# Performance work log

Hardware: AMD Instinct MI355X
Metric: run time of the kernel (lower is better)

## Reference

```python
import jax, jax.numpy as jnp
import numpy as np

NUM_EXPERTS = 8
TOP_K = 2
DIM = 1024
HIDDEN = 4096
B, S = 2, 1024


def setup_inputs() -> dict:
    key = jax.random.key(0)
    k_x, k_g, k_1, k_2, k_3 = jax.random.split(key, 5)
    s_d = 1.0 / np.sqrt(DIM)
    s_h = 1.0 / np.sqrt(HIDDEN)
    return {
        "x": jax.random.normal(k_x, (B, S, DIM), dtype=jnp.float32),
        "gate_w": jax.random.normal(k_g, (NUM_EXPERTS, DIM), dtype=jnp.float32) * s_d,
        "w1": jax.random.normal(k_1, (NUM_EXPERTS, HIDDEN, DIM), dtype=jnp.float32) * s_d,
        "w2": jax.random.normal(k_2, (NUM_EXPERTS, DIM, HIDDEN), dtype=jnp.float32) * s_h,
        "w3": jax.random.normal(k_3, (NUM_EXPERTS, HIDDEN, DIM), dtype=jnp.float32) * s_d,
    }


def reference(x, gate_w, w1, w2, w3):
    orig_shape = x.shape
    xt = x.reshape(-1, orig_shape[-1])                      # [T, D]
    scores = xt @ gate_w.T                                  # [T, E] (gate_softmax=False)
    top_vals, top_idx = jax.lax.top_k(scores, TOP_K)        # [T, K]
    top_w = jax.nn.softmax(top_vals, axis=-1)               # [T, K]
    # per-token combine weights over experts: [T, E]
    combine = jnp.einsum("tke,tk->te", jax.nn.one_hot(top_idx, NUM_EXPERTS, dtype=xt.dtype), top_w)
    # dense per-expert SwiGLU FFN; combine masks out unrouted experts
    h = jax.nn.silu(jnp.einsum("td,ehd->eth", xt, w1)) * jnp.einsum("td,ehd->eth", xt, w3)
    ye = jnp.einsum("eth,edh->etd", h, w2)                  # [E, T, D]
    y = jnp.einsum("te,etd->td", combine, ye)               # [T, D]
    return y.reshape(orig_shape)
```

## Files before the change

kernel.cpp:

```cpp
#include <hip/hip_runtime.h>
#include <hip/hip_bf16.h>

#define NUM_EXPERTS 8
#define TOPK 2
#define DIM 1024
#define HIDDEN 4096
#define T_TOKENS 2048
#define TOTAL_ROWS (T_TOKENS * TOPK)
#define LDSP 40

typedef __bf16 bf16x8 __attribute__((ext_vector_type(8)));
typedef float f32x4 __attribute__((ext_vector_type(4)));

__device__ __forceinline__ unsigned short f2bf(float f) {
  unsigned int u = __float_as_uint(f);
  u += 0x7FFF + ((u >> 16) & 1);
  return (unsigned short)(u >> 16);
}

__device__ __forceinline__ void gl_lds16(const void* g, void* l) {
  __builtin_amdgcn_global_load_lds(
      (const __attribute__((address_space(1))) unsigned int*)g,
      (__attribute__((address_space(3))) unsigned int*)l, 16, 0, 0);
}

#define WAIT_VM(N) __builtin_amdgcn_s_waitcnt(0x0F70 | (N))
#define BARRIER() __builtin_amdgcn_s_barrier()

__global__ __launch_bounds__(256) void cast_kernel(
    const float* __restrict__ src, unsigned short* __restrict__ dst, int n8) {
  int i = blockIdx.x * blockDim.x + threadIdx.x;
  int stride = gridDim.x * blockDim.x;
  for (; i < n8; i += stride) {
    float4 a = ((const float4*)src)[i * 2];
    float4 b = ((const float4*)src)[i * 2 + 1];
    ushort4 o0, o1;
    o0.x = f2bf(a.x); o0.y = f2bf(a.y); o0.z = f2bf(a.z); o0.w = f2bf(a.w);
    o1.x = f2bf(b.x); o1.y = f2bf(b.y); o1.z = f2bf(b.z); o1.w = f2bf(b.w);
    ((ushort4*)dst)[i * 2] = o0;
    ((ushort4*)dst)[i * 2 + 1] = o1;
  }
}

__global__ __launch_bounds__(256) void gate_kernel(
    const float* __restrict__ x, const float* __restrict__ gw,
    int* __restrict__ tok_idx, float* __restrict__ tok_w) {
  int wid = threadIdx.x >> 6;
  int lane = threadIdx.x & 63;
  int t = blockIdx.x * 4 + wid;
  if (t >= T_TOKENS) return;

  float xv[16];
#pragma unroll
  for (int i = 0; i < 16; i++) xv[i] = x[t * DIM + lane + i * 64];

  float s[NUM_EXPERTS];
#pragma unroll
  for (int e = 0; e < NUM_EXPERTS; e++) {
    float acc = 0.f;
#pragma unroll
    for (int i = 0; i < 16; i++) acc += xv[i] * gw[e * DIM + lane + i * 64];
#pragma unroll
    for (int off = 32; off; off >>= 1) acc += __shfl_xor(acc, off, 64);
    s[e] = acc;
  }
  if (lane == 0) {
    int i0 = 0;
    float v0 = s[0];
#pragma unroll
    for (int e = 1; e < NUM_EXPERTS; e++)
      if (s[e] > v0) { v0 = s[e]; i0 = e; }
    int i1 = -1;
    float v1 = -1e30f;
#pragma unroll
    for (int e = 0; e < NUM_EXPERTS; e++)
      if (e != i0 && s[e] > v1) { v1 = s[e]; i1 = e; }
    float e1 = __expf(v1 - v0);
    float d = 1.f + e1;
    tok_idx[t * 2] = i0;
    tok_idx[t * 2 + 1] = i1;
    tok_w[t * 2] = 1.f / d;
    tok_w[t * 2 + 1] = e1 / d;
  }
}

__global__ void scatter_kernel(const int* __restrict__ tok_idx,
                               const float* __restrict__ tok_w,
                               int* __restrict__ row_token,
                               float* __restrict__ row_weight,
                               int* __restrict__ counts,
                               int* __restrict__ offsets) {
  __shared__ int sc[NUM_EXPERTS];
  int tid = threadIdx.x;
  if (tid < NUM_EXPERTS) sc[tid] = 0;
  __syncthreads();
  for (int i = tid; i < TOTAL_ROWS; i += blockDim.x)
    atomicAdd(&sc[tok_idx[i]], 1);
  __syncthreads();
  if (tid == 0) {
    int run = 0;
    for (int e = 0; e < NUM_EXPERTS; e++) {
      int c = sc[e];
      counts[e] = c;
      offsets[e] = run;
      sc[e] = run;
      run += c;
    }
  }
  __syncthreads();
  for (int i = tid; i < TOTAL_ROWS; i += blockDim.x) {
    int e = tok_idx[i];
    int pos = atomicAdd(&sc[e], 1);
    row_token[pos] = i >> 1;
    row_weight[pos] = tok_w[i];
  }
}


__global__ __launch_bounds__(256) void ffn1_fast(
    const unsigned short* __restrict__ xb, const unsigned short* __restrict__ w1b,
    const unsigned short* __restrict__ w3b, const int* __restrict__ row_token,
    const int* __restrict__ counts, const int* __restrict__ offsets,
    unsigned short* __restrict__ hbuf) {
  int e = blockIdx.z;
  int cnt = counts[e];
  int m0 = blockIdx.y * 128;
  if (m0 >= cnt) return;
  int n0 = blockIdx.x * 128;
  int row_base = offsets[e];

  __shared__ __align__(16) unsigned short lA[2][128 * 32];
  __shared__ __align__(16) unsigned short lB1[2][128 * 32];
  __shared__ __align__(16) unsigned short lB3[2][128 * 32];

  int tid = threadIdx.x;
  int lane = tid & 63, wid = tid >> 6;
  int quad = lane >> 4, l16 = lane & 15;
  int wm = wid >> 1, wn = wid & 1;

  long aoff[2];
  long boff[2];
#pragma unroll
  for (int it = 0; it < 2; it++) {
    int c = it * 256 + tid;
    int r = c >> 2, seg = c & 3;
    int t = (m0 + r) < cnt ? row_token[row_base + m0 + r] : 0;
    aoff[it] = (long)t * DIM + seg * 8;
    boff[it] = (long)r * DIM + seg * 8;
  }
  const unsigned short* w1p = w1b + (long)e * HIDDEN * DIM + (long)n0 * DIM;
  const unsigned short* w3p = w3b + (long)e * HIDDEN * DIM + (long)n0 * DIM;

  f32x4 acc1[4][4], acc3[4][4];
#pragma unroll
  for (int mi = 0; mi < 4; mi++)
#pragma unroll
    for (int ni = 0; ni < 4; ni++) {
      acc1[mi][ni] = (f32x4){0.f, 0.f, 0.f, 0.f};
      acc3[mi][ni] = (f32x4){0.f, 0.f, 0.f, 0.f};
    }

#pragma unroll
  for (int it = 0; it < 2; it++) {
    int c = it * 256 + tid;
    gl_lds16(xb + aoff[it], &lA[0][c * 8]);
    gl_lds16(w1p + boff[it], &lB1[0][c * 8]);
    gl_lds16(w3p + boff[it], &lB3[0][c * 8]);
  }

  int pc = 0;
  for (int k0 = 0; k0 < DIM; k0 += 32, pc ^= 1) {
    BARRIER();
    if (k0 + 32 < DIM) {
      int nb = pc ^ 1, kn = k0 + 32;
#pragma unroll
      for (int it = 0; it < 2; it++) {
        int c = it * 256 + tid;
        gl_lds16(xb + aoff[it] + kn, &lA[nb][c * 8]);
        gl_lds16(w1p + boff[it] + kn, &lB1[nb][c * 8]);
        gl_lds16(w3p + boff[it] + kn, &lB3[nb][c * 8]);
      }
      WAIT_VM(6);
    } else {
      WAIT_VM(0);
    }
    BARRIER();

    bf16x8 af[4], b1f[4], b3f[4];
#pragma unroll
    for (int i = 0; i < 4; i++) {
      af[i]  = *(const bf16x8*)(const void*)&lA[pc][(wm * 64 + i * 16 + l16) * 32 + quad * 8];
      b1f[i] = *(const bf16x8*)(const void*)&lB1[pc][(wn * 64 + i * 16 + l16) * 32 + quad * 8];
      b3f[i] = *(const bf16x8*)(const void*)&lB3[pc][(wn * 64 + i * 16 + l16) * 32 + quad * 8];
    }
#pragma unroll
    for (int mi = 0; mi < 4; mi++)
#pragma unroll
      for (int ni = 0; ni < 4; ni++) {
        acc1[mi][ni] = __builtin_amdgcn_mfma_f32_16x16x32_bf16(af[mi], b1f[ni], acc1[mi][ni], 0, 0, 0);
        acc3[mi][ni] = __builtin_amdgcn_mfma_f32_16x16x32_bf16(af[mi], b3f[ni], acc3[mi][ni], 0, 0, 0);
      }
  }

#pragma unroll
  for (int mi = 0; mi < 4; mi++) {
#pragma unroll
    for (int r = 0; r < 4; r++) {
      int m = wm * 64 + mi * 16 + quad * 4 + r;
      if (m0 + m < cnt) {
        long rowoff = (long)(row_base + m0 + m) * HIDDEN;
#pragma unroll
        for (int ni = 0; ni < 4; ni++) {
          int n = n0 + wn * 64 + ni * 16 + l16;
          float v1 = acc1[mi][ni][r];
          float v3 = acc3[mi][ni][r];
          float sig = 1.f / (1.f + __expf(-v1));
          hbuf[rowoff + n] = f2bf(v1 * sig * v3);
        }
      }
    }
  }
}

__global__ __launch_bounds__(256) void ffn2_fast(
    const unsigned short* __restrict__ hbuf, const unsigned short* __restrict__ w2b,
    const int* __restrict__ row_token, const float* __restrict__ row_weight,
    const int* __restrict__ counts, const int* __restrict__ offsets,
    float* __restrict__ y) {
  int e = blockIdx.z;
  int cnt = counts[e];
  int mt = blockIdx.y >> 1, kh = blockIdx.y & 1;
  int m0 = mt * 128;
  if (m0 >= cnt) return;
  int n0 = blockIdx.x * 128;
  int row_base = offsets[e];
  const int KHALF = HIDDEN / 2;
  int kbeg = kh * KHALF;

  __shared__ __align__(16) unsigned short lA[2][128 * 32];
  __shared__ __align__(16) unsigned short lB[2][128 * 32];

  int tid = threadIdx.x;
  int lane = tid & 63, wid = tid >> 6;
  int quad = lane >> 4, l16 = lane & 15;
  int wm = wid >> 1, wn = wid & 1;

  long aoff[2], boff[2];
#pragma unroll
  for (int it = 0; it < 2; it++) {
    int c = it * 256 + tid;
    int r = c >> 2, seg = c & 3;
    int row = (m0 + r) < cnt ? (row_base + m0 + r) : row_base;
    aoff[it] = (long)row * HIDDEN + seg * 8 + kbeg;
    boff[it] = (long)r * HIDDEN + seg * 8 + kbeg;
  }
  const unsigned short* w2p = w2b + (long)e * DIM * HIDDEN + (long)n0 * HIDDEN;

  f32x4 acc[4][4];
#pragma unroll
  for (int mi = 0; mi < 4; mi++)
#pragma unroll
    for (int ni = 0; ni < 4; ni++) acc[mi][ni] = (f32x4){0.f, 0.f, 0.f, 0.f};

#pragma unroll
  for (int it = 0; it < 2; it++) {
    int c = it * 256 + tid;
    gl_lds16(hbuf + aoff[it], &lA[0][c * 8]);
    gl_lds16(w2p + boff[it], &lB[0][c * 8]);
  }

  int pc = 0;
  for (int k0 = 0; k0 < KHALF; k0 += 32, pc ^= 1) {
    BARRIER();
    if (k0 + 32 < KHALF) {
      int nb = pc ^ 1, kn = k0 + 32;
#pragma unroll
      for (int it = 0; it < 2; it++) {
        int c = it * 256 + tid;
        gl_lds16(hbuf + aoff[it] + kn, &lA[nb][c * 8]);
        gl_lds16(w2p + boff[it] + kn, &lB[nb][c * 8]);
      }
      WAIT_VM(4);
    } else {
      WAIT_VM(0);
    }
    BARRIER();

    bf16x8 af[4], bfr[4];
#pragma unroll
    for (int i = 0; i < 4; i++) {
      af[i]  = *(const bf16x8*)(const void*)&lA[pc][(wm * 64 + i * 16 + l16) * 32 + quad * 8];
      bfr[i] = *(const bf16x8*)(const void*)&lB[pc][(wn * 64 + i * 16 + l16) * 32 + quad * 8];
    }
#pragma unroll
    for (int mi = 0; mi < 4; mi++)
#pragma unroll
      for (int ni = 0; ni < 4; ni++)
        acc[mi][ni] = __builtin_amdgcn_mfma_f32_16x16x32_bf16(af[mi], bfr[ni], acc[mi][ni], 0, 0, 0);
  }

#pragma unroll
  for (int mi = 0; mi < 4; mi++) {
#pragma unroll
    for (int r = 0; r < 4; r++) {
      int m = wm * 64 + mi * 16 + quad * 4 + r;
      if (m0 + m < cnt) {
        int t = row_token[row_base + m0 + m];
        float wgt = row_weight[row_base + m0 + m];
        long yoff = (long)t * DIM + n0 + wn * 64;
#pragma unroll
        for (int ni = 0; ni < 4; ni++)
          atomicAdd(&y[yoff + ni * 16 + l16], wgt * acc[mi][ni][r]);
      }
    }
  }
}


__global__ __launch_bounds__(256) void ffn1_slow(
    const float* __restrict__ x, const float* __restrict__ w1,
    const float* __restrict__ w3, const int* __restrict__ row_token,
    const int* __restrict__ counts, const int* __restrict__ offsets,
    unsigned short* __restrict__ hbuf) {
  int e = blockIdx.z;
  int cnt = counts[e];
  int m0 = blockIdx.y * 128;
  if (m0 >= cnt) return;
  int n0 = blockIdx.x * 128;
  int row_base = offsets[e];

  __shared__ __align__(16) unsigned short lA[128 * LDSP];
  __shared__ __align__(16) unsigned short lB1[128 * LDSP];
  __shared__ __align__(16) unsigned short lB3[128 * LDSP];

  int tid = threadIdx.x;
  int lane = tid & 63, wid = tid >> 6;
  int quad = lane >> 4, l16 = lane & 15;
  int wm = wid >> 1, wn = wid & 1;

  long aoff[4];
  bool aval[4];
#pragma unroll
  for (int it = 0; it < 4; it++) {
    int linear = it * 256 + tid;
    int r = linear >> 3, c4 = linear & 7;
    bool v = (m0 + r) < cnt;
    aval[it] = v;
    int t = v ? row_token[row_base + m0 + r] : 0;
    aoff[it] = (long)t * DIM + c4 * 4;
  }
  const float* w1p = w1 + (long)e * HIDDEN * DIM;
  const float* w3p = w3 + (long)e * HIDDEN * DIM;

  f32x4 acc1[4][4], acc3[4][4];
#pragma unroll
  for (int mi = 0; mi < 4; mi++)
#pragma unroll
    for (int ni = 0; ni < 4; ni++) {
      acc1[mi][ni] = (f32x4){0.f, 0.f, 0.f, 0.f};
      acc3[mi][ni] = (f32x4){0.f, 0.f, 0.f, 0.f};
    }

  for (int k0 = 0; k0 < DIM; k0 += 32) {
#pragma unroll
    for (int it = 0; it < 4; it++) {
      int linear = it * 256 + tid;
      int r = linear >> 3, c4 = linear & 7;
      float4 v = make_float4(0.f, 0.f, 0.f, 0.f);
      if (aval[it]) v = *(const float4*)(x + aoff[it] + k0);
      ushort4 b;
      b.x = f2bf(v.x); b.y = f2bf(v.y); b.z = f2bf(v.z); b.w = f2bf(v.w);
      *(ushort4*)&lA[r * LDSP + c4 * 4] = b;
    }
#pragma unroll
    for (int it = 0; it < 4; it++) {
      int linear = it * 256 + tid;
      int r = linear >> 3, c4 = linear & 7;
      long boff = (long)(n0 + r) * DIM + k0 + c4 * 4;
      float4 v1 = *(const float4*)(w1p + boff);
      float4 v3 = *(const float4*)(w3p + boff);
      ushort4 b1, b3;
      b1.x = f2bf(v1.x); b1.y = f2bf(v1.y); b1.z = f2bf(v1.z); b1.w = f2bf(v1.w);
      b3.x = f2bf(v3.x); b3.y = f2bf(v3.y); b3.z = f2bf(v3.z); b3.w = f2bf(v3.w);
      *(ushort4*)&lB1[r * LDSP + c4 * 4] = b1;
      *(ushort4*)&lB3[r * LDSP + c4 * 4] = b3;
    }
    __syncthreads();

    bf16x8 af[4], b1f[4], b3f[4];
#pragma unroll
    for (int i = 0; i < 4; i++) {
      af[i]  = *(const bf16x8*)(const void*)&lA[(wm * 64 + i * 16 + l16) * LDSP + quad * 8];
      b1f[i] = *(const bf16x8*)(const void*)&lB1[(wn * 64 + i * 16 + l16) * LDSP + quad * 8];
      b3f[i] = *(const bf16x8*)(const void*)&lB3[(wn * 64 + i * 16 + l16) * LDSP + quad * 8];
    }
#pragma unroll
    for (int mi = 0; mi < 4; mi++)
#pragma unroll
      for (int ni = 0; ni < 4; ni++) {
        acc1[mi][ni] = __builtin_amdgcn_mfma_f32_16x16x32_bf16(af[mi], b1f[ni], acc1[mi][ni], 0, 0, 0);
        acc3[mi][ni] = __builtin_amdgcn_mfma_f32_16x16x32_bf16(af[mi], b3f[ni], acc3[mi][ni], 0, 0, 0);
      }
    __syncthreads();
  }

#pragma unroll
  for (int mi = 0; mi < 4; mi++) {
#pragma unroll
    for (int r = 0; r < 4; r++) {
      int m = wm * 64 + mi * 16 + quad * 4 + r;
      if (m0 + m < cnt) {
        long rowoff = (long)(row_base + m0 + m) * HIDDEN;
#pragma unroll
        for (int ni = 0; ni < 4; ni++) {
          int n = n0 + wn * 64 + ni * 16 + l16;
          float v1 = acc1[mi][ni][r];
          float v3 = acc3[mi][ni][r];
          float sig = 1.f / (1.f + __expf(-v1));
          hbuf[rowoff + n] = f2bf(v1 * sig * v3);
        }
      }
    }
  }
}

__global__ __launch_bounds__(256) void ffn2_slow(
    const unsigned short* __restrict__ hbuf, const float* __restrict__ w2,
    const int* __restrict__ row_token, const float* __restrict__ row_weight,
    const int* __restrict__ counts, const int* __restrict__ offsets,
    float* __restrict__ y) {
  int e = blockIdx.z;
  int cnt = counts[e];
  int m0 = blockIdx.y * 128;
  if (m0 >= cnt) return;
  int n0 = blockIdx.x * 128;
  int row_base = offsets[e];

  __shared__ __align__(16) unsigned short lA[128 * LDSP];
  __shared__ __align__(16) unsigned short lB[128 * LDSP];

  int tid = threadIdx.x;
  int lane = tid & 63, wid = tid >> 6;
  int quad = lane >> 4, l16 = lane & 15;
  int wm = wid >> 1, wn = wid & 1;

  const float* w2p = w2 + (long)e * DIM * HIDDEN;

  f32x4 acc[4][4];
#pragma unroll
  for (int mi = 0; mi < 4; mi++)
#pragma unroll
    for (int ni = 0; ni < 4; ni++) acc[mi][ni] = (f32x4){0.f, 0.f, 0.f, 0.f};

  for (int k0 = 0; k0 < HIDDEN; k0 += 32) {
#pragma unroll
    for (int it = 0; it < 2; it++) {
      int linear = it * 256 + tid;
      int r = linear >> 2, c8 = linear & 3;
      float4 v = make_float4(0.f, 0.f, 0.f, 0.f);
      if (m0 + r < cnt)
        v = *(const float4*)(hbuf + (long)(row_base + m0 + r) * HIDDEN + k0 + c8 * 8);
      *(float4*)&lA[r * LDSP + c8 * 8] = v;
    }
#pragma unroll
    for (int it = 0; it < 4; it++) {
      int linear = it * 256 + tid;
      int r = linear >> 3, c4 = linear & 7;
      float4 v = *(const float4*)(w2p + (long)(n0 + r) * HIDDEN + k0 + c4 * 4);
      ushort4 b;
      b.x = f2bf(v.x); b.y = f2bf(v.y); b.z = f2bf(v.z); b.w = f2bf(v.w);
      *(ushort4*)&lB[r * LDSP + c4 * 4] = b;
    }
    __syncthreads();

    bf16x8 af[4], bfr[4];
#pragma unroll
    for (int i = 0; i < 4; i++) {
      af[i]  = *(const bf16x8*)(const void*)&lA[(wm * 64 + i * 16 + l16) * LDSP + quad * 8];
      bfr[i] = *(const bf16x8*)(const void*)&lB[(wn * 64 + i * 16 + l16) * LDSP + quad * 8];
    }
#pragma unroll
    for (int mi = 0; mi < 4; mi++)
#pragma unroll
      for (int ni = 0; ni < 4; ni++)
        acc[mi][ni] = __builtin_amdgcn_mfma_f32_16x16x32_bf16(af[mi], bfr[ni], acc[mi][ni], 0, 0, 0);
    __syncthreads();
  }

#pragma unroll
  for (int mi = 0; mi < 4; mi++) {
#pragma unroll
    for (int r = 0; r < 4; r++) {
      int m = wm * 64 + mi * 16 + quad * 4 + r;
      if (m0 + m < cnt) {
        int t = row_token[row_base + m0 + m];
        float wgt = row_weight[row_base + m0 + m];
        long yoff = (long)t * DIM + n0 + wn * 64;
#pragma unroll
        for (int ni = 0; ni < 4; ni++)
          atomicAdd(&y[yoff + ni * 16 + l16], wgt * acc[mi][ni][r]);
      }
    }
  }
}

extern "C" void kernel_launch(void* const* d_in, const int* in_sizes, int n_in,
                              void* d_out, int out_size, void* d_ws, size_t ws_size,
                              hipStream_t stream) {
  const float* x = (const float*)d_in[0];
  const float* gw = (const float*)d_in[1];
  const float* w1 = (const float*)d_in[2];
  const float* w2 = (const float*)d_in[3];
  const float* w3 = (const float*)d_in[4];
  float* y = (float*)d_out;

  char* ws = (char*)d_ws;
  int* row_token = (int*)ws;
  float* row_weight = (float*)(ws + 16384);
  int* counts = (int*)(ws + 32768);
  int* offsets = (int*)(ws + 32768 + 32);
  int* tok_idx = (int*)(ws + 32896);
  float* tok_w = (float*)(ws + 32896 + 16384);
  const size_t HBUF_OFF = 65664;
  const size_t XB_OFF   = HBUF_OFF + 33554432ull;
  const size_t W1B_OFF  = XB_OFF + 4194304ull;
  const size_t W2B_OFF  = W1B_OFF + 67108864ull;
  const size_t W3B_OFF  = W2B_OFF + 67108864ull;
  const size_t NEED     = W3B_OFF + 67108864ull;
  unsigned short* hbuf = (unsigned short*)(ws + HBUF_OFF);

  hipMemsetAsync(d_out, 0, (size_t)T_TOKENS * DIM * sizeof(float), stream);
  gate_kernel<<<T_TOKENS / 4, 256, 0, stream>>>(x, gw, tok_idx, tok_w);
  scatter_kernel<<<1, 256, 0, stream>>>(tok_idx, tok_w, row_token, row_weight, counts, offsets);

  if (ws_size >= NEED) {
    unsigned short* xb  = (unsigned short*)(ws + XB_OFF);
    unsigned short* w1b = (unsigned short*)(ws + W1B_OFF);
    unsigned short* w2b = (unsigned short*)(ws + W2B_OFF);
    unsigned short* w3b = (unsigned short*)(ws + W3B_OFF);
    const int NW8 = NUM_EXPERTS * HIDDEN * DIM / 8;
    cast_kernel<<<512, 256, 0, stream>>>(x, xb, T_TOKENS * DIM / 8);
    cast_kernel<<<2048, 256, 0, stream>>>(w1, w1b, NW8);
    cast_kernel<<<2048, 256, 0, stream>>>(w3, w3b, NW8);
    cast_kernel<<<2048, 256, 0, stream>>>(w2, w2b, NW8);
    ffn1_fast<<<dim3(HIDDEN / 128, TOTAL_ROWS / 128, NUM_EXPERTS), 256, 0, stream>>>(
        xb, w1b, w3b, row_token, counts, offsets, hbuf);
    ffn2_fast<<<dim3(DIM / 128, (TOTAL_ROWS / 128) * 2, NUM_EXPERTS), 256, 0, stream>>>(
        hbuf, w2b, row_token, row_weight, counts, offsets, y);
  } else {
    ffn1_slow<<<dim3(HIDDEN / 128, TOTAL_ROWS / 128, NUM_EXPERTS), 256, 0, stream>>>(
        x, w1, w3, row_token, counts, offsets, hbuf);
    ffn2_slow<<<dim3(DIM / 128, TOTAL_ROWS / 128, NUM_EXPERTS), 256, 0, stream>>>(
        hbuf, w2, row_token, row_weight, counts, offsets, y);
  }
}
```

Baseline: 694.4 us.

## Compact expert tile list, pre-gather token rows, split FFN2 K four ways

The scatter kernel now emits a compact list of (expert, m0) tiles, so both FFN kernels launch over only the tiles that exist instead of a full expert-by-maximum-tile grid where most blocks exit early. Token rows are gathered and cast to bf16 in routed order before FFN1, so its A loads read contiguous rows instead of doing indirect token lookups. FFN2 splits K into quarters rather than halves to give more blocks, at the cost of more atomic accumulation into the output. The x cast kernel is replaced by the gather kernel.

```diff
diff --git a/kernel.cpp b/kernel.cpp
--- a/kernel.cpp
+++ b/kernel.cpp
@@ -7,6 +7,7 @@
 #define HIDDEN 4096
 #define T_TOKENS 2048
 #define TOTAL_ROWS (T_TOKENS * TOPK)
+#define MAXTILES 40
 #define LDSP 40
 
 typedef __bf16 bf16x8 __attribute__((ext_vector_type(8)));
@@ -42,6 +43,24 @@
   }
 }
 
+__global__ __launch_bounds__(256) void xgather_kernel(
+    const float* __restrict__ x, const int* __restrict__ row_token,
+    unsigned short* __restrict__ xg) {
+  int half = threadIdx.x >> 7;
+  int lane = threadIdx.x & 127;
+  int row = blockIdx.x * 2 + half;
+  if (row >= TOTAL_ROWS) return;
+  int t = row_token[row];
+  const float4* src = (const float4*)(x + (long)t * DIM) + lane * 2;
+  float4 a = src[0], b = src[1];
+  ushort4 o0, o1;
+  o0.x = f2bf(a.x); o0.y = f2bf(a.y); o0.z = f2bf(a.z); o0.w = f2bf(a.w);
+  o1.x = f2bf(b.x); o1.y = f2bf(b.y); o1.z = f2bf(b.z); o1.w = f2bf(b.w);
+  ushort4* dst = (ushort4*)(xg + (long)row * DIM) + lane * 2;
+  dst[0] = o0;
+  dst[1] = o1;
+}
+
 __global__ __launch_bounds__(256) void gate_kernel(
     const float* __restrict__ x, const float* __restrict__ gw,
     int* __restrict__ tok_idx, float* __restrict__ tok_w) {
@@ -89,7 +108,10 @@
                                int* __restrict__ row_token,
                                float* __restrict__ row_weight,
                                int* __restrict__ counts,
-                               int* __restrict__ offsets) {
+                               int* __restrict__ offsets,
+                               int* __restrict__ tile_e,
+                               int* __restrict__ tile_m0,
+                               int* __restrict__ ntiles) {
   __shared__ int sc[NUM_EXPERTS];
   int tid = threadIdx.x;
   if (tid < NUM_EXPERTS) sc[tid] = 0;
@@ -98,14 +120,20 @@
     atomicAdd(&sc[tok_idx[i]], 1);
   __syncthreads();
   if (tid == 0) {
-    int run = 0;
+    int run = 0, nt = 0;
     for (int e = 0; e < NUM_EXPERTS; e++) {
       int c = sc[e];
       counts[e] = c;
       offsets[e] = run;
+      for (int m0 = 0; m0 < c; m0 += 128) {
+        tile_e[nt] = e;
+        tile_m0[nt] = m0;
+        nt++;
+      }
       sc[e] = run;
       run += c;
     }
+    *ntiles = nt;
   }
   __syncthreads();
   for (int i = tid; i < TOTAL_ROWS; i += blockDim.x) {
@@ -118,16 +146,19 @@
 
 
 __global__ __launch_bounds__(256) void ffn1_fast(
-    const unsigned short* __restrict__ xb, const unsigned short* __restrict__ w1b,
-    const unsigned short* __restrict__ w3b, const int* __restrict__ row_token,
+    const unsigned short* __restrict__ xg, const unsigned short* __restrict__ w1b,
+    const unsigned short* __restrict__ w3b,
+    const int* __restrict__ tile_e, const int* __restrict__ tile_m0,
+    const int* __restrict__ ntiles,
     const int* __restrict__ counts, const int* __restrict__ offsets,
     unsigned short* __restrict__ hbuf) {
-  int e = blockIdx.z;
+  int ty = blockIdx.y;
+  if (ty >= *ntiles) return;
+  int e = tile_e[ty];
+  int m0 = tile_m0[ty];
   int cnt = counts[e];
-  int m0 = blockIdx.y * 128;
-  if (m0 >= cnt) return;
+  int row_base = offsets[e];
   int n0 = blockIdx.x * 128;
-  int row_base = offsets[e];
 
   __shared__ __align__(16) unsigned short lA[2][128 * 32];
   __shared__ __align__(16) unsigned short lB1[2][128 * 32];
@@ -138,14 +169,14 @@
   int quad = lane >> 4, l16 = lane & 15;
   int wm = wid >> 1, wn = wid & 1;
 
-  long aoff[2];
-  long boff[2];
+  long aoff[2], boff[2];
 #pragma unroll
   for (int it = 0; it < 2; it++) {
     int c = it * 256 + tid;
     int r = c >> 2, seg = c & 3;
-    int t = (m0 + r) < cnt ? row_token[row_base + m0 + r] : 0;
-    aoff[it] = (long)t * DIM + seg * 8;
+    int rr = row_base + m0 + r;
+    if (rr > TOTAL_ROWS - 1) rr = TOTAL_ROWS - 1;
+    aoff[it] = (long)rr * DIM + seg * 8;
     boff[it] = (long)r * DIM + seg * 8;
   }
   const unsigned short* w1p = w1b + (long)e * HIDDEN * DIM + (long)n0 * DIM;
@@ -163,7 +194,7 @@
 #pragma unroll
   for (int it = 0; it < 2; it++) {
     int c = it * 256 + tid;
-    gl_lds16(xb + aoff[it], &lA[0][c * 8]);
+    gl_lds16(xg + aoff[it], &lA[0][c * 8]);
     gl_lds16(w1p + boff[it], &lB1[0][c * 8]);
     gl_lds16(w3p + boff[it], &lB3[0][c * 8]);
   }
@@ -176,7 +207,7 @@
 #pragma unroll
       for (int it = 0; it < 2; it++) {
         int c = it * 256 + tid;
-        gl_lds16(xb + aoff[it] + kn, &lA[nb][c * 8]);
+        gl_lds16(xg + aoff[it] + kn, &lA[nb][c * 8]);
         gl_lds16(w1p + boff[it] + kn, &lB1[nb][c * 8]);
         gl_lds16(w3p + boff[it] + kn, &lB3[nb][c * 8]);
       }
@@ -224,18 +255,20 @@
 
 __global__ __launch_bounds__(256) void ffn2_fast(
     const unsigned short* __restrict__ hbuf, const unsigned short* __restrict__ w2b,
+    const int* __restrict__ tile_e, const int* __restrict__ tile_m0,
+    const int* __restrict__ ntiles,
     const int* __restrict__ row_token, const float* __restrict__ row_weight,
     const int* __restrict__ counts, const int* __restrict__ offsets,
     float* __restrict__ y) {
-  int e = blockIdx.z;
+  int t4 = blockIdx.y >> 2, kh = blockIdx.y & 3;
+  if (t4 >= *ntiles) return;
+  int e = tile_e[t4];
+  int m0 = tile_m0[t4];
   int cnt = counts[e];
-  int mt = blockIdx.y >> 1, kh = blockIdx.y & 1;
-  int m0 = mt * 128;
-  if (m0 >= cnt) return;
+  int row_base = offsets[e];
   int n0 = blockIdx.x * 128;
-  int row_base = offsets[e];
-  const int KHALF = HIDDEN / 2;
-  int kbeg = kh * KHALF;
+  const int KQ = HIDDEN / 4;
+  int kbeg = kh * KQ;
 
   __shared__ __align__(16) unsigned short lA[2][128 * 32];
   __shared__ __align__(16) unsigned short lB[2][128 * 32];
@@ -250,8 +283,9 @@
   for (int it = 0; it < 2; it++) {
     int c = it * 256 + tid;
     int r = c >> 2, seg = c & 3;
-    int row = (m0 + r) < cnt ? (row_base + m0 + r) : row_base;
-    aoff[it] = (long)row * HIDDEN + seg * 8 + kbeg;
+    int rr = row_base + m0 + r;
+    if (rr > TOTAL_ROWS - 1) rr = TOTAL_ROWS - 1;
+    aoff[it] = (long)rr * HIDDEN + seg * 8 + kbeg;
     boff[it] = (long)r * HIDDEN + seg * 8 + kbeg;
   }
   const unsigned short* w2p = w2b + (long)e * DIM * HIDDEN + (long)n0 * HIDDEN;
@@ -270,9 +304,9 @@
   }
 
   int pc = 0;
-  for (int k0 = 0; k0 < KHALF; k0 += 32, pc ^= 1) {
+  for (int k0 = 0; k0 < KQ; k0 += 32, pc ^= 1) {
     BARRIER();
-    if (k0 + 32 < KHALF) {
+    if (k0 + 32 < KQ) {
       int nb = pc ^ 1, kn = k0 + 32;
 #pragma unroll
       for (int it = 0; it < 2; it++) {
@@ -518,12 +552,15 @@
   int* row_token = (int*)ws;
   float* row_weight = (float*)(ws + 16384);
   int* counts = (int*)(ws + 32768);
-  int* offsets = (int*)(ws + 32768 + 32);
-  int* tok_idx = (int*)(ws + 32896);
-  float* tok_w = (float*)(ws + 32896 + 16384);
-  const size_t HBUF_OFF = 65664;
-  const size_t XB_OFF   = HBUF_OFF + 33554432ull;
-  const size_t W1B_OFF  = XB_OFF + 4194304ull;
+  int* offsets = (int*)(ws + 32800);
+  int* tile_e = (int*)(ws + 32832);
+  int* tile_m0 = (int*)(ws + 33088);
+  int* ntiles = (int*)(ws + 33344);
+  int* tok_idx = (int*)(ws + 33408);
+  float* tok_w = (float*)(ws + 49792);
+  const size_t HBUF_OFF = 66560;
+  const size_t XG_OFF   = HBUF_OFF + 33554432ull;
+  const size_t W1B_OFF  = XG_OFF + 8388608ull;
   const size_t W2B_OFF  = W1B_OFF + 67108864ull;
   const size_t W3B_OFF  = W2B_OFF + 67108864ull;
   const size_t NEED     = W3B_OFF + 67108864ull;
@@ -531,22 +568,23 @@
 
   hipMemsetAsync(d_out, 0, (size_t)T_TOKENS * DIM * sizeof(float), stream);
   gate_kernel<<<T_TOKENS / 4, 256, 0, stream>>>(x, gw, tok_idx, tok_w);
-  scatter_kernel<<<1, 256, 0, stream>>>(tok_idx, tok_w, row_token, row_weight, counts, offsets);
+  scatter_kernel<<<1, 256, 0, stream>>>(tok_idx, tok_w, row_token, row_weight,
+                                        counts, offsets, tile_e, tile_m0, ntiles);
 
   if (ws_size >= NEED) {
-    unsigned short* xb  = (unsigned short*)(ws + XB_OFF);
+    unsigned short* xg  = (unsigned short*)(ws + XG_OFF);
     unsigned short* w1b = (unsigned short*)(ws + W1B_OFF);
     unsigned short* w2b = (unsigned short*)(ws + W2B_OFF);
     unsigned short* w3b = (unsigned short*)(ws + W3B_OFF);
     const int NW8 = NUM_EXPERTS * HIDDEN * DIM / 8;
-    cast_kernel<<<512, 256, 0, stream>>>(x, xb, T_TOKENS * DIM / 8);
+    xgather_kernel<<<TOTAL_ROWS / 2, 256, 0, stream>>>(x, row_token, xg);
     cast_kernel<<<2048, 256, 0, stream>>>(w1, w1b, NW8);
     cast_kernel<<<2048, 256, 0, stream>>>(w3, w3b, NW8);
     cast_kernel<<<2048, 256, 0, stream>>>(w2, w2b, NW8);
-    ffn1_fast<<<dim3(HIDDEN / 128, TOTAL_ROWS / 128, NUM_EXPERTS), 256, 0, stream>>>(
-        xb, w1b, w3b, row_token, counts, offsets, hbuf);
-    ffn2_fast<<<dim3(DIM / 128, (TOTAL_ROWS / 128) * 2, NUM_EXPERTS), 256, 0, stream>>>(
-        hbuf, w2b, row_token, row_weight, counts, offsets, y);
+    ffn1_fast<<<dim3(HIDDEN / 128, MAXTILES), 256, 0, stream>>>(
+        xg, w1b, w3b, tile_e, tile_m0, ntiles, counts, offsets, hbuf);
+    ffn2_fast<<<dim3(DIM / 128, MAXTILES * 4), 256, 0, stream>>>(
+        hbuf, w2b, tile_e, tile_m0, ntiles, row_token, row_weight, counts, offsets, y);
   } else {
     ffn1_slow<<<dim3(HIDDEN / 128, TOTAL_ROWS / 128, NUM_EXPERTS), 256, 0, stream>>>(
         x, w1, w3, row_token, counts, offsets, hbuf);
```

After: 716.6 us. 3.2% more time.
